# Kernel tuning notes

Measured on AMD Instinct MI355X. Metric: run time of the kernel, lower is better.

Reference implementation:

```python
import jax, jax.numpy as jnp
import numpy as np

N_HEADS = 16
N_KV = 8
HEAD_DIM = 128
HID = 2048
GROUPS = N_HEADS // N_KV
THETA = 10000.0


def _rope_cos_sin(position_ids, dtype):
    # position_ids: [1, S] int
    inv_freq = 1.0 / (THETA ** (jnp.arange(0, HEAD_DIM, 2, dtype=jnp.float32) / HEAD_DIM))
    freqs = position_ids.astype(jnp.float32)[:, :, None] * inv_freq[None, None, :]  # [1,S,hd/2]
    emb = jnp.concatenate([freqs, freqs], axis=-1)  # [1,S,hd]
    return jnp.cos(emb).astype(dtype)[:, None, :, :], jnp.sin(emb).astype(dtype)[:, None, :, :]


def _rotate_half(x):
    x1, x2 = x[..., : HEAD_DIM // 2], x[..., HEAD_DIM // 2 :]
    return jnp.concatenate([-x2, x1], axis=-1)


def setup_inputs() -> dict:
    key = jax.random.key(0)
    ks = jax.random.split(key, 8)
    B, S = 2, 2048
    hidden_states = jax.random.normal(ks[0], (B, S, HID), jnp.float32)
    Wq = jax.random.normal(ks[1], (HID, N_HEADS * HEAD_DIM), jnp.float32) * 0.02
    Wk = jax.random.normal(ks[2], (HID, N_KV * HEAD_DIM), jnp.float32) * 0.02
    Wv = jax.random.normal(ks[3], (HID, N_KV * HEAD_DIM), jnp.float32) * 0.02
    Wo = jax.random.normal(ks[4], (HID, HID), jnp.float32) * 0.02
    gate = jnp.zeros((1, N_HEADS, 1, 1), jnp.float32)
    memory_in = jax.random.normal(ks[5], (B, N_KV, HEAD_DIM, HEAD_DIM), jnp.float32)
    norm_in = jax.random.uniform(ks[6], (B, N_KV, 1, HEAD_DIM), jnp.float32)
    position_ids = jnp.arange(S, dtype=jnp.int32)[None, :]
    return {"hidden_states": hidden_states, "Wq": Wq, "Wk": Wk, "Wv": Wv, "Wo": Wo,
            "gate": gate, "memory_in": memory_in, "norm_in": norm_in,
            "position_ids": position_ids}


def reference(hidden_states, Wq, Wk, Wv, Wo, gate, memory_in, norm_in, position_ids):
    B, S, _ = hidden_states.shape
    # projections -> [B, H, S, hd]
    q = jnp.einsum('bsh,ho->bso', hidden_states, Wq).reshape(B, S, N_HEADS, HEAD_DIM).transpose(0, 2, 1, 3)
    k = jnp.einsum('bsh,ho->bso', hidden_states, Wk).reshape(B, S, N_KV, HEAD_DIM).transpose(0, 2, 1, 3)
    v = jnp.einsum('bsh,ho->bso', hidden_states, Wv).reshape(B, S, N_KV, HEAD_DIM).transpose(0, 2, 1, 3)

    # ---- compressive memory retrieval (pre-RoPE q, as in original) ----
    sigma_q = jax.nn.elu(q) + 1.0  # [B, nH, S, hd]
    mem_tiled = jnp.tile(memory_in, (1, GROUPS, 1, 1))          # torch .repeat tiles
    norm_tiled = jnp.tile(norm_in, (1, GROUPS, 1, 1))            # [B, nH, 1, hd]
    memory_output = jnp.einsum('bhsd,bhde->bhse', sigma_q, mem_tiled)
    norm_bcast = jnp.einsum('bhsd,bhd->bhs', sigma_q, norm_tiled[:, :, 0, :])[..., None]
    memory_output = memory_output / norm_bcast

    # ---- memory update (pre-RoPE k, v) ----
    sigma_k = jax.nn.elu(k) + 1.0  # [B, nKV, S, hd]
    updated_memory = memory_in + jnp.einsum('bhsd,bhse->bhde', sigma_k, v)
    updated_norm = norm_in + jnp.sum(sigma_k, axis=2, keepdims=True)

    # ---- RoPE ----
    cos, sin = _rope_cos_sin(position_ids, q.dtype)
    q = q * cos + _rotate_half(q) * sin
    k = k * cos + _rotate_half(k) * sin

    # ---- repeat_kv (interleave, groups) ----
    k = jnp.repeat(k, GROUPS, axis=1)
    v = jnp.repeat(v, GROUPS, axis=1)

    # ---- causal SDPA ----
    scale = 1.0 / np.sqrt(HEAD_DIM)
    scores = jnp.einsum('bhqd,bhkd->bhqk', q, k) * scale
    causal = jnp.tril(jnp.ones((S, S), dtype=bool))
    scores = jnp.where(causal[None, None], scores, jnp.finfo(scores.dtype).min)
    probs = jax.nn.softmax(scores, axis=-1)
    attn = jnp.einsum('bhqk,bhkd->bhqd', probs, v)

    # ---- gated combination + output projection ----
    g = jax.nn.sigmoid(gate)
    combined = g * memory_output + (1.0 - g) * attn  # [B, nH, S, hd]
    combined = combined.transpose(0, 2, 1, 3).reshape(B, S, HID)
    final_output = jnp.einsum('bsh,ho->bso', combined, Wo)
    return final_output, updated_memory, updated_norm
```

## Files before the change

kernel.cpp:

```cpp
#include <hip/hip_runtime.h>

#define BATCH 2
#define SEQ   2048
#define HID   2048
#define NH    16
#define NKV   8
#define HD    128
#define M_ROWS (BATCH * SEQ)
#define QKV_N  4096

typedef __attribute__((ext_vector_type(8))) __bf16 bf16x8;
typedef __attribute__((ext_vector_type(4))) float  f32x4;

static __device__ __forceinline__ f32x4 mfma16(bf16x8 a, bf16x8 b, f32x4 c) {
    return __builtin_amdgcn_mfma_f32_16x16x32_bf16(a, b, c, 0, 0, 0);
}
static __device__ __forceinline__ float sigma_f(float x) {
    return x > 0.f ? x + 1.f : __expf(x);
}
static __device__ __forceinline__ void gload16(const __bf16* g, __bf16* l) {
    __builtin_amdgcn_global_load_lds(
        (const __attribute__((address_space(1))) void*)g,
        (__attribute__((address_space(3))) void*)l, 16, 0, 0);
}

#define OFF_QKV  0ull
#define OFF_SQ   67108864ull
#define OFF_QR   83886080ull
#define OFF_KR   100663296ull
#define OFF_VT   109051904ull
#define OFF_ND   117440512ull
#define OFF_CB   117702656ull
#define OFF_PART 134479872ull
#define OFF_BND  142868480ull
#define OFF_MAXP 143130624ull
#define OFF_NPART 143134720ull
#define NSPLIT 8

__global__ void f2b_k(const float* __restrict__ src, __bf16* __restrict__ dst)
{
    const size_t i = ((size_t)blockIdx.x * 256 + threadIdx.x) * 8;
    const float4 v0 = *reinterpret_cast<const float4*>(src + i);
    const float4 v1 = *reinterpret_cast<const float4*>(src + i + 4);
    bf16x8 t;
    t[0]=(__bf16)v0.x; t[1]=(__bf16)v0.y; t[2]=(__bf16)v0.z; t[3]=(__bf16)v0.w;
    t[4]=(__bf16)v1.x; t[5]=(__bf16)v1.y; t[6]=(__bf16)v1.z; t[7]=(__bf16)v1.w;
    *reinterpret_cast<bf16x8*>(dst + i) = t;
}

__global__ __launch_bounds__(256) void tr_k(const float* __restrict__ W,
                                            __bf16* __restrict__ Bt, int K, int N)
{
    __shared__ __bf16 T[64][72];
    const int k0 = blockIdx.x * 64, n0 = blockIdx.y * 64;
    const int t = threadIdx.x;
    #pragma unroll
    for (int i = 0; i < 4; ++i) {
        const int idx = t + i * 256;
        const int r = idx >> 4, c4 = (idx & 15) * 4;
        const float4 v = *reinterpret_cast<const float4*>(&W[(size_t)(k0 + r) * N + n0 + c4]);
        T[c4 + 0][r] = (__bf16)v.x; T[c4 + 1][r] = (__bf16)v.y;
        T[c4 + 2][r] = (__bf16)v.z; T[c4 + 3][r] = (__bf16)v.w;
    }
    __syncthreads();
    #pragma unroll
    for (int i = 0; i < 2; ++i) {
        const int idx = t + i * 256;
        const int rr = idx >> 3, cc = (idx & 7) * 8;
        *reinterpret_cast<bf16x8*>(&Bt[(size_t)(n0 + rr) * K + k0 + cc]) =
            *reinterpret_cast<bf16x8*>(&T[rr][cc]);
    }
}

__global__ __launch_bounds__(512, 2) void gemm8_k(const __bf16* __restrict__ A,
                                                  const __bf16* __restrict__ Bt,
                                                  float* __restrict__ C,
                                                  int N, int K)
{
    __shared__ __align__(16) __bf16 smem[65536];
    const int tid = threadIdx.x, wave = tid >> 6, lane = tid & 63;
    const int l15 = lane & 15, l4 = lane >> 4;
    const int wr = wave >> 2, wc = wave & 3;

    const int nwg = gridDim.x;
    const int swz = (blockIdx.x & 7) * (nwg >> 3) + (blockIdx.x >> 3);
    const int NBN = N >> 8;
    const int bm = swz / NBN, bn = swz - bm * NBN;
    const int m0 = bm << 8, n0 = bn << 8;

    const int NKT = K >> 6;

    const int srow   = tid >> 2;
    const int schunk = (tid & 3) ^ ((tid >> 3) & 3);
    const int sdst   = wave * 512;

    const int achunk = l4 ^ ((l15 >> 1) & 3);
    const int aoff = (wr * 128 + l15) * 32 + achunk * 8;
    const int boff = (wc * 64  + l15) * 32 + achunk * 8;

    f32x4 acc[2][4][4] = {};
    bf16x8 af[4], bfr[4];

#define STAGE_SLAB(gb, r0, koff, slabptr) do {                                   \
        const __bf16* _g = (gb) + (size_t)((r0) + srow) * K + (koff) + schunk * 8; \
        gload16(_g,                    (slabptr) + sdst);                        \
        gload16(_g + (size_t)128 * K,  (slabptr) + sdst + 4096);                 \
    } while (0)

    STAGE_SLAB(A,  m0, 0,  smem);
    STAGE_SLAB(Bt, n0, 0,  smem + 16384);
    STAGE_SLAB(A,  m0, 32, smem + 8192);
    STAGE_SLAB(Bt, n0, 32, smem + 24576);
    STAGE_SLAB(A,  m0, 64, smem + 32768);
    STAGE_SLAB(Bt, n0, 64, smem + 32768 + 16384);
    asm volatile("s_waitcnt vmcnt(4)" ::: "memory");
    __builtin_amdgcn_s_barrier();

    #pragma unroll 1
    for (int T = 0; T < NKT; ++T) {
        __bf16* bufc = smem + (T & 1) * 32768;
        __bf16* bufn = smem + ((T & 1) ^ 1) * 32768;
        const int kt1 = (T + 1) * 64, kt2 = (T + 2) * 64;

        {
            const __bf16* As = bufc;
            const __bf16* Bs = bufc + 16384;
            #pragma unroll
            for (int f = 0; f < 4; ++f)  af[f]  = *reinterpret_cast<const bf16x8*>(As + aoff + f * 512);
            #pragma unroll
            for (int nf = 0; nf < 4; ++nf) bfr[nf] = *reinterpret_cast<const bf16x8*>(Bs + boff + nf * 512);
            if (T + 1 < NKT) STAGE_SLAB(A, m0, kt1 + 32, bufn + 8192);
            __builtin_amdgcn_s_barrier();
            __builtin_amdgcn_s_setprio(1);
            #pragma unroll
            for (int f = 0; f < 4; ++f)
                #pragma unroll
                for (int nf = 0; nf < 4; ++nf)
                    acc[0][f][nf] = mfma16(af[f], bfr[nf], acc[0][f][nf]);
            __builtin_amdgcn_s_setprio(0);
            __builtin_amdgcn_s_barrier();
        }
        {
            const __bf16* As = bufc;
            #pragma unroll
            for (int f = 0; f < 4; ++f)  af[f] = *reinterpret_cast<const bf16x8*>(As + aoff + 2048 + f * 512);
            if (T + 1 < NKT) STAGE_SLAB(Bt, n0, kt1 + 32, bufn + 24576);
            __builtin_amdgcn_s_barrier();
            __builtin_amdgcn_s_setprio(1);
            #pragma unroll
            for (int f = 0; f < 4; ++f)
                #pragma unroll
                for (int nf = 0; nf < 4; ++nf)
                    acc[1][f][nf] = mfma16(af[f], bfr[nf], acc[1][f][nf]);
            __builtin_amdgcn_s_setprio(0);
            __builtin_amdgcn_s_barrier();
        }
        {
            const __bf16* As = bufc + 8192;
            const __bf16* Bs = bufc + 24576;
            #pragma unroll
            for (int f = 0; f < 4; ++f)  af[f]  = *reinterpret_cast<const bf16x8*>(As + aoff + f * 512);
            #pragma unroll
            for (int nf = 0; nf < 4; ++nf) bfr[nf] = *reinterpret_cast<const bf16x8*>(Bs + boff + nf * 512);
            if (T + 2 < NKT) STAGE_SLAB(A, m0, kt2, bufc);
            __builtin_amdgcn_s_barrier();
            __builtin_amdgcn_s_setprio(1);
            #pragma unroll
            for (int f = 0; f < 4; ++f)
                #pragma unroll
                for (int nf = 0; nf < 4; ++nf)
                    acc[0][f][nf] = mfma16(af[f], bfr[nf], acc[0][f][nf]);
            __builtin_amdgcn_s_setprio(0);
            __builtin_amdgcn_s_barrier();
        }
        {
            const __bf16* As = bufc + 8192;
            #pragma unroll
            for (int f = 0; f < 4; ++f)  af[f] = *reinterpret_cast<const bf16x8*>(As + aoff + 2048 + f * 512);
            if (T + 2 < NKT) STAGE_SLAB(Bt, n0, kt2, bufc + 16384);
            __builtin_amdgcn_s_barrier();
            __builtin_amdgcn_s_setprio(1);
            #pragma unroll
            for (int f = 0; f < 4; ++f)
                #pragma unroll
                for (int nf = 0; nf < 4; ++nf)
                    acc[1][f][nf] = mfma16(af[f], bfr[nf], acc[1][f][nf]);
            __builtin_amdgcn_s_setprio(0);
            if (T < NKT - 2) asm volatile("s_waitcnt vmcnt(4)" ::: "memory");
            else             asm volatile("s_waitcnt vmcnt(0)" ::: "memory");
            __builtin_amdgcn_s_barrier();
        }
    }
#undef STAGE_SLAB

    #pragma unroll
    for (int mh = 0; mh < 2; ++mh)
        #pragma unroll
        for (int f = 0; f < 4; ++f)
            #pragma unroll
            for (int nf = 0; nf < 4; ++nf)
                #pragma unroll
                for (int r = 0; r < 4; ++r) {
                    const int row = m0 + wr * 128 + mh * 64 + f * 16 + l4 * 4 + r;
                    const int col = n0 + wc * 64 + nf * 16 + l15;
                    C[(size_t)row * N + col] = acc[mh][f][nf][r];
                }
}

__global__ __launch_bounds__(256) void prep_k(const float* __restrict__ qkv,
                                              const float* __restrict__ norm_in,
                                              const int* __restrict__ pos_ids,
                                              __bf16* __restrict__ sq, __bf16* __restrict__ qr,
                                              __bf16* __restrict__ kr, __bf16* __restrict__ vt,
                                              float* __restrict__ nd, float* __restrict__ bnd,
                                              float* __restrict__ maxp)
{
    const int sc = blockIdx.x, kvh = blockIdx.y, b = blockIdx.z;
    const int s0 = sc * 32, t = threadIdx.x;
    const float scale = 0.08838834764831845f;
    const float s2 = scale * scale;
    const float NEG_LN_TH = -0.14391156831212787f;
    __shared__ float krn[32];

    {
        const int row = t >> 2;
        const int head = row >> 5, sl = row & 31;
        const int hq = kvh * 2 + head, nh = hq & 7;
        const int dq = (t & 3) * 16;
        const int pos = pos_ids[s0 + sl];
        const float* qp = qkv + (size_t)(b * SEQ + s0 + sl) * QKV_N + hq * 128;
        const float* np = norm_in + (b * NKV + nh) * 128;

        float x0[16], x1[16];
        #pragma unroll
        for (int i = 0; i < 16; i += 4) {
            *reinterpret_cast<float4*>(&x0[i]) = *reinterpret_cast<const float4*>(qp + dq + i);
            *reinterpret_cast<float4*>(&x1[i]) = *reinterpret_cast<const float4*>(qp + dq + 64 + i);
        }
        float nds = 0.f, qns = 0.f;
        bf16x8 sqv0[2], sqv1[2], qrv0[2], qrv1[2];
        #pragma unroll
        for (int i = 0; i < 16; ++i) {
            const int j = dq + i;
            float c, sn;
            __sincosf((float)pos * __expf((float)j * NEG_LN_TH), &sn, &c);
            qrv0[i >> 3][i & 7] = (__bf16)((x0[i] * c - x1[i] * sn) * scale);
            qrv1[i >> 3][i & 7] = (__bf16)((x1[i] * c + x0[i] * sn) * scale);
            const float sg0 = sigma_f(x0[i]), sg1 = sigma_f(x1[i]);
            sqv0[i >> 3][i & 7] = (__bf16)sg0;
            sqv1[i >> 3][i & 7] = (__bf16)sg1;
            nds += sg0 * np[j] + sg1 * np[j + 64];
            qns += (x0[i] * x0[i] + x1[i] * x1[i]) * s2;
        }
        __bf16* sqp = sq + ((size_t)(b * NH + hq) * SEQ + s0 + sl) * 128;
        __bf16* qrp = qr + ((size_t)(b * NH + hq) * SEQ + s0 + sl) * 128;
        *reinterpret_cast<bf16x8*>(sqp + dq)      = sqv0[0];
        *reinterpret_cast<bf16x8*>(sqp + dq + 8)  = sqv0[1];
        *reinterpret_cast<bf16x8*>(sqp + dq + 64) = sqv1[0];
        *reinterpret_cast<bf16x8*>(sqp + dq + 72) = sqv1[1];
        *reinterpret_cast<bf16x8*>(qrp + dq)      = qrv0[0];
        *reinterpret_cast<bf16x8*>(qrp + dq + 8)  = qrv0[1];
        *reinterpret_cast<bf16x8*>(qrp + dq + 64) = qrv1[0];
        *reinterpret_cast<bf16x8*>(qrp + dq + 72) = qrv1[1];

        nds += __shfl_xor(nds, 1); nds += __shfl_xor(nds, 2);
        qns += __shfl_xor(qns, 1); qns += __shfl_xor(qns, 2);
        if ((t & 3) == 0) {
            nd [(size_t)(b * NH + hq) * SEQ + s0 + sl] = nds;
            bnd[(size_t)(b * NH + hq) * SEQ + s0 + sl] = qns;
        }
    }

    if (t < 128) {
        const int sl = t >> 2;
        const int dq = (t & 3) * 16;
        const int pos = pos_ids[s0 + sl];
        const float* kp = qkv + (size_t)(b * SEQ + s0 + sl) * QKV_N + 2048 + kvh * 128;
        float x0[16], x1[16];
        #pragma unroll
        for (int i = 0; i < 16; i += 4) {
            *reinterpret_cast<float4*>(&x0[i]) = *reinterpret_cast<const float4*>(kp + dq + i);
            *reinterpret_cast<float4*>(&x1[i]) = *reinterpret_cast<const float4*>(kp + dq + 64 + i);
        }
        bf16x8 kv0[2], kv1[2];
        float kns = 0.f;
        #pragma unroll
        for (int i = 0; i < 16; ++i) {
            const int j = dq + i;
            float c, sn;
            __sincosf((float)pos * __expf((float)j * NEG_LN_TH), &sn, &c);
            kv0[i >> 3][i & 7] = (__bf16)(x0[i] * c - x1[i] * sn);
            kv1[i >> 3][i & 7] = (__bf16)(x1[i] * c + x0[i] * sn);
            kns += x0[i] * x0[i] + x1[i] * x1[i];
        }
        __bf16* krp = kr + ((size_t)(b * NKV + kvh) * SEQ + s0 + sl) * 128;
        *reinterpret_cast<bf16x8*>(krp + dq)      = kv0[0];
        *reinterpret_cast<bf16x8*>(krp + dq + 8)  = kv0[1];
        *reinterpret_cast<bf16x8*>(krp + dq + 64) = kv1[0];
        *reinterpret_cast<bf16x8*>(krp + dq + 72) = kv1[1];
        kns += __shfl_xor(kns, 1); kns += __shfl_xor(kns, 2);
        if ((t & 3) == 0) krn[sl] = kns;
    }

    __shared__ float vl[128][33];
    {
        const int sl = t >> 3, dch = (t & 7) * 16;
        const float* vp = qkv + (size_t)(b * SEQ + s0 + sl) * QKV_N + 3072 + kvh * 128 + dch;
        float xv[16];
        #pragma unroll
        for (int i = 0; i < 16; i += 4)
            *reinterpret_cast<float4*>(&xv[i]) = *reinterpret_cast<const float4*>(vp + i);
        #pragma unroll
        for (int i = 0; i < 16; ++i) vl[dch + i][sl] = xv[i];
    }
    __syncthreads();
    if (t == 0) {
        float mx = 0.f;
        #pragma unroll
        for (int i = 0; i < 32; ++i) mx = fmaxf(mx, krn[i]);
        maxp[((b * NKV + kvh) << 6) + sc] = mx;
    }
    {
        const int d = t >> 1, sh = (t & 1) * 16;
        bf16x8 o0, o1;
        #pragma unroll
        for (int j = 0; j < 8; ++j) o0[j] = (__bf16)vl[d][sh + j];
        #pragma unroll
        for (int j = 0; j < 8; ++j) o1[j] = (__bf16)vl[d][sh + 8 + j];
        __bf16* vp = vt + ((size_t)((b * NKV + kvh) * 128 + d)) * SEQ + s0 + sh;
        *reinterpret_cast<bf16x8*>(vp)     = o0;
        *reinterpret_cast<bf16x8*>(vp + 8) = o1;
    }
}

__global__ __launch_bounds__(256) void memout_k(const __bf16* __restrict__ sq,
                                                const float* __restrict__ mem_in,
                                                const float* __restrict__ nd,
                                                const float* __restrict__ gate,
                                                __bf16* __restrict__ cb)
{
    __shared__ __align__(16) __bf16 mt[128][136];
    const int tid = threadIdx.x;
    const int h = blockIdx.y, b = blockIdx.z;
    const int s0 = blockIdx.x * 64;

    const float* mem = mem_in + (size_t)(b * NKV + (h & 7)) * 16384;
    for (int i = tid; i < 16384; i += 256) {
        int dd = i >> 7, e = i & 127;
        mt[e][dd] = (__bf16)mem[i];
    }
    __syncthreads();

    const int wave = tid >> 6, lane = tid & 63, l15 = lane & 15, l4 = lane >> 4;
    f32x4 acc[8] = {};
    const __bf16* sqb = sq + ((size_t)(b * NH + h) * SEQ + s0 + wave * 16 + l15) * 128;
    #pragma unroll
    for (int kb = 0; kb < 4; ++kb) {
        bf16x8 a = *reinterpret_cast<const bf16x8*>(sqb + kb * 32 + l4 * 8);
        #pragma unroll
        for (int nc = 0; nc < 8; ++nc) {
            bf16x8 bb = *reinterpret_cast<bf16x8*>(&mt[nc * 16 + l15][kb * 32 + l4 * 8]);
            acc[nc] = mfma16(a, bb, acc[nc]);
        }
    }
    float g = 1.f / (1.f + __expf(-gate[h]));
    #pragma unroll
    for (int r = 0; r < 4; ++r) {
        int srow = s0 + wave * 16 + l4 * 4 + r;
        float scl = g / nd[(size_t)(b * NH + h) * SEQ + srow];
        __bf16* cbp = cb + (size_t)(b * SEQ + srow) * HID + h * 128;
        #pragma unroll
        for (int nc = 0; nc < 8; ++nc)
            cbp[nc * 16 + l15] = (__bf16)(acc[nc][r] * scl);
    }
}

__global__ __launch_bounds__(256) void memupd_k(const float* __restrict__ qkv,
                                                float* __restrict__ part,
                                                float* __restrict__ npart)
{
    const int sp = blockIdx.x, h = blockIdx.y, b = blockIdx.z;
    const int tid = threadIdx.x;
    const int tx = tid & 15, ty = tid >> 4;
    __shared__ __align__(16) float sk[8][128];
    __shared__ __align__(16) float sv[8][128];
    float acc[8][8] = {};
    float nacc = 0.f;

    const int s0 = sp * (SEQ / NSPLIT);
    for (int so = 0; so < SEQ / NSPLIT; so += 8) {
        for (int i = tid; i < 8 * 128; i += 256) {
            int rr = i >> 7, dd = i & 127;
            const float* rowp = qkv + (size_t)(b * SEQ + s0 + so + rr) * QKV_N;
            sk[rr][dd] = sigma_f(rowp[2048 + h * 128 + dd]);
            sv[rr][dd] = rowp[3072 + h * 128 + dd];
        }
        __syncthreads();
        if (tid < 128) {
            #pragma unroll
            for (int rr = 0; rr < 8; ++rr) nacc += sk[rr][tid];
        }
        #pragma unroll
        for (int rr = 0; rr < 8; ++rr) {
            float4 k0 = *reinterpret_cast<float4*>(&sk[rr][tx * 8]);
            float4 k1 = *reinterpret_cast<float4*>(&sk[rr][tx * 8 + 4]);
            float4 v0 = *reinterpret_cast<float4*>(&sv[rr][ty * 8]);
            float4 v1 = *reinterpret_cast<float4*>(&sv[rr][ty * 8 + 4]);
            float kreg[8] = {k0.x,k0.y,k0.z,k0.w,k1.x,k1.y,k1.z,k1.w};
            float vreg[8] = {v0.x,v0.y,v0.z,v0.w,v1.x,v1.y,v1.z,v1.w};
            #pragma unroll
            for (int i = 0; i < 8; ++i)
                #pragma unroll
                for (int j2 = 0; j2 < 8; ++j2)
                    acc[i][j2] += kreg[i] * vreg[j2];
        }
        __syncthreads();
    }
    float* pb = part + ((size_t)sp * (BATCH * NKV) + b * NKV + h) * 16384;
    #pragma unroll
    for (int i = 0; i < 8; ++i)
        #pragma unroll
        for (int j2 = 0; j2 < 8; ++j2)
            pb[(tx * 8 + i) * 128 + ty * 8 + j2] = acc[i][j2];
    if (tid < 128)
        npart[((size_t)sp * (BATCH * NKV) + b * NKV + h) * 128 + tid] = nacc;
}

__global__ void memred_k(const float* __restrict__ part, const float* __restrict__ mem_in,
                         float* __restrict__ out_mem)
{
    const size_t i = (size_t)blockIdx.x * 256 + threadIdx.x;
    float a = mem_in[i];
    #pragma unroll
    for (int sp = 0; sp < NSPLIT; ++sp) a += part[(size_t)sp * 262144 + i];
    out_mem[i] = a;
}

__global__ void normred_k(const float* __restrict__ npart, const float* __restrict__ norm_in,
                          float* __restrict__ out_norm)
{
    const int bh = blockIdx.x, d = threadIdx.x;
    float a = norm_in[bh * 128 + d];
    #pragma unroll
    for (int sp = 0; sp < NSPLIT; ++sp)
        a += npart[((size_t)sp * (BATCH * NKV) + bh) * 128 + d];
    out_norm[bh * 128 + d] = a;
}

__global__ __launch_bounds__(256, 2) void attn_k(const __bf16* __restrict__ qr,
                                                 const __bf16* __restrict__ kr,
                                                 const __bf16* __restrict__ vt,
                                                 const float* __restrict__ gate,
                                                 const float* __restrict__ bnd,
                                                 const float* __restrict__ maxp,
                                                 __bf16* __restrict__ cb)
{
    __shared__ __align__(16) char smem[81920];
    char* ksB = smem;
    char* vsB = smem + 32768;
    char* pB  = smem + 65536;
    float*  red  = (float*)smem;
    float*  lred = (float*)(smem + 65536);

    const int tid = threadIdx.x, wave = tid >> 6, lane = tid & 63;
    const int l15 = lane & 15, l4 = lane >> 4;
    const int e3 = l15 & 7, e2 = e3 >> 2;
    const int ksub = wave >> 1;
    const int wq   = wave & 1;

    const int n   = blockIdx.x + 16 * (blockIdx.y + 16 * blockIdx.z);
    const int xcd = n & 7, i64 = n >> 3;
    const int grp = xcd * 2 + (i64 >> 5);
    const int within = i64 & 31;
    const int b   = grp >> 3;
    const int kvh = grp & 7;
    const int h   = kvh * 2 + (within >> 4);
    const int x   = within & 15;

    const __bf16* kbase = kr + (size_t)(b * NKV + kvh) * SEQ * 128;
    const __bf16* vbase = vt + (size_t)(b * NKV + kvh) * 128 * SEQ;
    const float* bbase  = bnd + (size_t)(b * NH + h) * SEQ;

    const float g  = 1.f / (1.f + __expf(-gate[h]));
    const float gi = 1.f - g;
    float kn2 = 0.f;
    const float* mp = maxp + (b * NKV + kvh) * 64;
    #pragma unroll
    for (int i = 0; i < 64; i += 4) {
        const float4 v = *reinterpret_cast<const float4*>(mp + i);
        kn2 = fmaxf(kn2, fmaxf(fmaxf(v.x, v.y), fmaxf(v.z, v.w)));
    }
    const float knmax = sqrtf(kn2);

    bf16x8 ones;
    #pragma unroll
    for (int j = 0; j < 8; ++j) ones[j] = (__bf16)1.0f;

    const int srow = wave * 32 + l4;
    const int chA  = (lane & 15) ^ l4;
    const char* KG0 = (const char*)kbase + srow * 256 + chA * 16;
    const char* KG1 = (const char*)kbase + srow * 256 + ((chA ^ 4) * 16);
    const char* VG0 = (const char*)vbase + srow * 4096 + chA * 16;
    const char* VG1 = (const char*)vbase + srow * 4096 + ((chA ^ 4) * 16);
    __bf16* kdst = (__bf16*)(ksB + wave * 8192);
    __bf16* vdst = (__bf16*)(vsB + wave * 8192);

    const int t16 = (l4 ^ (e3 & 3)) * 16;
    const int KBe = l15 * 256 + ksub * 16384 + t16 + e2 * 64;
    const int KBo = l15 * 256 + ksub * 16384 + t16 + (1 ^ e2) * 64;
    const int VB0 = l15 * 256 + t16 + e2 * 64 + ksub * 128;
    const int VB1 = l15 * 256 + t16 + (1 ^ e2) * 64 + ksub * 128;
    const int PWw = wave * 4096 + l4 * 512 + l15 * 2;
    const int PWr = wave * 4096 + l15 * 128 + l4 * 16;

#define ISSUE_K(ktrow) do {                                                      \
        const int _ko = (ktrow) * 256;                                           \
        _Pragma("unroll")                                                        \
        for (int _j = 0; _j < 8; ++_j)                                           \
            gload16((const __bf16*)(((_j & 1) ? KG1 : KG0) + _ko + _j * 1024),   \
                    kdst + _j * 512);                                            \
    } while (0)
#define ISSUE_V(ktrow) do {                                                      \
        const int _vo = (ktrow) * 2;                                             \
        _Pragma("unroll")                                                        \
        for (int _j = 0; _j < 8; ++_j)                                           \
            gload16((const __bf16*)(((_j & 1) ? VG1 : VG0) + _vo + _j * 16384),  \
                    vdst + _j * 512);                                            \
    } while (0)

    #pragma unroll 1
    for (int tile = 0; tile < 2; ++tile) {
        const int q0 = (tile == 0 ? x : 31 - x) * 64;
        const int qw = q0 + wq * 32;
        const int NT = (q0 >> 6) + 1;
        const int NI = (NT + 1) >> 1;

        bf16x8 af[2][4];
        float m_r[2][4];
        #pragma unroll
        for (int m = 0; m < 2; ++m) {
            const __bf16* qb = qr + ((size_t)(b * NH + h) * SEQ + qw + m * 16 + l15) * 128;
            #pragma unroll
            for (int kb = 0; kb < 4; ++kb)
                af[m][kb] = *reinterpret_cast<const bf16x8*>(qb + kb * 32 + l4 * 8);
            #pragma unroll
            for (int r = 0; r < 4; ++r)
                m_r[m][r] = sqrtf(bbase[qw + m * 16 + l4 * 4 + r]) * knmax + 1.0f;
        }

        f32x4 o0[8] = {}, o1[8] = {};
        f32x4 lc0 = {}, lc1 = {};

        ISSUE_K(0);
        ISSUE_V(0);
        asm volatile("s_waitcnt vmcnt(8)" ::: "memory");
        __builtin_amdgcn_sched_barrier(0);
        __builtin_amdgcn_s_barrier();

        #pragma unroll 1
        for (int it = 0; it < NI; ++it) {
            const int s = 2 * it + ksub;
            const bool act  = (s < NT);
            const bool more = (it + 1 < NI);

            f32x4 s0[4] = {}, s1[4] = {};
            if (act) {
                __builtin_amdgcn_s_setprio(1);
                #pragma unroll
                for (int kb = 0; kb < 4; ++kb) {
                    const int kbb = ((kb & 1) ? KBo : KBe) + (kb >> 1) * 128;
                    #pragma unroll
                    for (int sub = 0; sub < 4; ++sub) {
                        bf16x8 bb = *reinterpret_cast<const bf16x8*>(ksB + kbb + sub * 4096);
                        s0[sub] = mfma16(af[0][kb], bb, s0[sub]);
                        s1[sub] = mfma16(af[1][kb], bb, s1[sub]);
                    }
                }
                __builtin_amdgcn_s_setprio(0);
            }
            __builtin_amdgcn_sched_barrier(0);
            __builtin_amdgcn_s_barrier();

            if (more) ISSUE_K((it + 1) * 128);

            if (act) {
                #pragma unroll
                for (int r = 0; r < 4; ++r) {
                    const int q0r = qw + l4 * 4 + r;
                    const int q1r = q0r + 16;
                    #pragma unroll
                    for (int sub = 0; sub < 4; ++sub) {
                        const int key = s * 64 + sub * 16 + l15;
                        float p0 = __expf(s0[sub][r] - m_r[0][r]);
                        float p1 = __expf(s1[sub][r] - m_r[1][r]);
                        p0 = (key <= q0r) ? p0 : 0.f;
                        p1 = (key <= q1r) ? p1 : 0.f;
                        *(__bf16*)(pB + PWw + r * 128 + sub * 32)        = (__bf16)p0;
                        *(__bf16*)(pB + PWw + 2048 + r * 128 + sub * 32) = (__bf16)p1;
                    }
                }
            }
            if (more) asm volatile("s_waitcnt vmcnt(8)" ::: "memory");
            else      asm volatile("s_waitcnt vmcnt(0)" ::: "memory");
            __builtin_amdgcn_sched_barrier(0);
            __builtin_amdgcn_s_barrier();

            if (act) {
                bf16x8 a00 = *reinterpret_cast<const bf16x8*>(pB + PWr);
                bf16x8 a01 = *reinterpret_cast<const bf16x8*>(pB + PWr + 64);
                bf16x8 a10 = *reinterpret_cast<const bf16x8*>(pB + PWr + 2048);
                bf16x8 a11 = *reinterpret_cast<const bf16x8*>(pB + PWr + 2048 + 64);
                __builtin_amdgcn_s_setprio(1);
                lc0 = mfma16(a00, ones, lc0); lc0 = mfma16(a01, ones, lc0);
                lc1 = mfma16(a10, ones, lc1); lc1 = mfma16(a11, ones, lc1);
                #pragma unroll
                for (int nc = 0; nc < 8; ++nc) {
                    bf16x8 b0 = *reinterpret_cast<const bf16x8*>(vsB + VB0 + nc * 4096);
                    bf16x8 b1 = *reinterpret_cast<const bf16x8*>(vsB + VB1 + nc * 4096);
                    o0[nc] = mfma16(a00, b0, o0[nc]); o0[nc] = mfma16(a01, b1, o0[nc]);
                    o1[nc] = mfma16(a10, b0, o1[nc]); o1[nc] = mfma16(a11, b1, o1[nc]);
                }
                __builtin_amdgcn_s_setprio(0);
            }
            __builtin_amdgcn_sched_barrier(0);
            __builtin_amdgcn_s_barrier();

            if (more) {
                ISSUE_V((it + 1) * 128);
                asm volatile("s_waitcnt vmcnt(8)" ::: "memory");
            } else {
                asm volatile("s_waitcnt vmcnt(0)" ::: "memory");
            }
            __builtin_amdgcn_sched_barrier(0);
            __builtin_amdgcn_s_barrier();
        }

        if (wave >= 2) {
            float* rb = red + (wave - 2) * 4224;
            #pragma unroll
            for (int nc = 0; nc < 8; ++nc)
                #pragma unroll
                for (int r = 0; r < 4; ++r) {
                    rb[(l4 * 4 + r) * 132 + nc * 16 + l15]        = o0[nc][r];
                    rb[(16 + l4 * 4 + r) * 132 + nc * 16 + l15]   = o1[nc][r];
                }
            if (l15 == 0) {
                float* lb = lred + (wave - 2) * 32;
                #pragma unroll
                for (int r = 0; r < 4; ++r) {
                    lb[l4 * 4 + r]      = lc0[r];
                    lb[16 + l4 * 4 + r] = lc1[r];
                }
            }
        }
        __syncthreads();
        if (wave < 2) {
            float* rb = red + wave * 4224;
            const float* lb = lred + wave * 32;
            #pragma unroll
            for (int r = 0; r < 4; ++r) {
                const int qrow = qw + l4 * 4 + r;
                const float i0 = gi / (lc0[r] + lb[l4 * 4 + r]);
                const float i1 = gi / (lc1[r] + lb[16 + l4 * 4 + r]);
                __bf16* c0 = cb + (size_t)(b * SEQ + qrow) * HID + h * 128;
                __bf16* c1 = cb + (size_t)(b * SEQ + qrow + 16) * HID + h * 128;
                #pragma unroll
                for (int nc = 0; nc < 8; ++nc) {
                    const int dd = nc * 16 + l15;
                    const float v0 = o0[nc][r] + rb[(l4 * 4 + r) * 132 + dd];
                    const float v1 = o1[nc][r] + rb[(16 + l4 * 4 + r) * 132 + dd];
                    c0[dd] = (__bf16)((float)c0[dd] + v0 * i0);
                    c1[dd] = (__bf16)((float)c1[dd] + v1 * i1);
                }
            }
        }
        __syncthreads();
    }
#undef ISSUE_K
#undef ISSUE_V
}

extern "C" void kernel_launch(void* const* d_in, const int* in_sizes, int n_in,
                              void* d_out, int out_size, void* d_ws, size_t ws_size,
                              hipStream_t stream)
{
    const float* hidden  = (const float*)d_in[0];
    const float* Wq      = (const float*)d_in[1];
    const float* Wk      = (const float*)d_in[2];
    const float* Wv      = (const float*)d_in[3];
    const float* Wo      = (const float*)d_in[4];
    const float* gate    = (const float*)d_in[5];
    const float* mem_in  = (const float*)d_in[6];
    const float* norm_in = (const float*)d_in[7];
    const int*   pos     = (const int*)d_in[8];

    float* out_final = (float*)d_out;
    float* out_mem   = out_final + (size_t)BATCH * SEQ * HID;
    float* out_norm  = out_mem + (size_t)BATCH * NKV * 128 * 128;

    char* ws = (char*)d_ws;
    float*  qkv  = (float*)(ws + OFF_QKV);
    __bf16* sq   = (__bf16*)(ws + OFF_SQ);
    __bf16* qrb  = (__bf16*)(ws + OFF_QR);
    __bf16* krb  = (__bf16*)(ws + OFF_KR);
    __bf16* vtb  = (__bf16*)(ws + OFF_VT);
    float*  nd   = (float*)(ws + OFF_ND);
    __bf16* cb   = (__bf16*)(ws + OFF_CB);
    float*  part = (float*)(ws + OFF_PART);
    float*  bnd  = (float*)(ws + OFF_BND);
    float*  maxp = (float*)(ws + OFF_MAXP);
    float*  npart = (float*)(ws + OFF_NPART);
    __bf16* hb   = (__bf16*)(ws + OFF_SQ);
    __bf16* qkvT = (__bf16*)(ws + OFF_QR);
    __bf16* woT  = (__bf16*)(ws + OFF_PART);

    f2b_k<<<(M_ROWS * HID) / (256 * 8), 256, 0, stream>>>(hidden, hb);
    tr_k<<<dim3(HID / 64, 2048 / 64), 256, 0, stream>>>(Wq, qkvT, HID, 2048);
    tr_k<<<dim3(HID / 64, 1024 / 64), 256, 0, stream>>>(Wk, qkvT + (size_t)2048 * HID, HID, 1024);
    tr_k<<<dim3(HID / 64, 1024 / 64), 256, 0, stream>>>(Wv, qkvT + (size_t)3072 * HID, HID, 1024);

    gemm8_k<<<(M_ROWS / 256) * (QKV_N / 256), 512, 0, stream>>>(hb, qkvT, qkv, QKV_N, HID);

    prep_k<<<dim3(SEQ / 32, NKV, BATCH), 256, 0, stream>>>(qkv, norm_in, pos, sq, qrb, krb, vtb,
                                                           nd, bnd, maxp);

    memout_k<<<dim3(SEQ / 64, NH, BATCH), 256, 0, stream>>>(sq, mem_in, nd, gate, cb);

    memupd_k<<<dim3(NSPLIT, NKV, BATCH), 256, 0, stream>>>(qkv, part, npart);
    memred_k<<<(BATCH * NKV * 128 * 128) / 256, 256, 0, stream>>>(part, mem_in, out_mem);
    normred_k<<<BATCH * NKV, 128, 0, stream>>>(npart, norm_in, out_norm);

    tr_k<<<dim3(HID / 64, HID / 64), 256, 0, stream>>>(Wo, woT, HID, HID);

    attn_k<<<dim3(16, NH, BATCH), 256, 0, stream>>>(qrb, krb, vtb, gate, bnd, maxp, cb);

    gemm8_k<<<(M_ROWS / 256) * (HID / 256), 512, 0, stream>>>(cb, woT, out_final, HID, HID);
}
```

Before: 470.3 us.

## Merge prep kernels, swizzle P tile in LDS, add smaller-tile output GEMM

Folds the hidden-state bf16 conversion and the three weight transposes into one launch, and merges the memory and norm reductions into another, cutting kernel launches. Applies an XOR swizzle to the attention probability tile in LDS to reduce bank conflicts on writes and reads. Replaces the output projection GEMM with a 128x256 tile variant with a blockIdx swizzle, double-buffered LDS and 2 blocks per CU, so the grid has more workgroups for better CU occupancy. The new GEMM adds another hand-written pipeline with waitcnt-based synchronisation that has to be correct.

```diff
diff --git a/kernel.cpp b/kernel.cpp
--- a/kernel.cpp
+++ b/kernel.cpp
@@ -37,15 +37,48 @@
 #define OFF_NPART 143134720ull
 #define NSPLIT 8
 
-__global__ void f2b_k(const float* __restrict__ src, __bf16* __restrict__ dst)
-{
-    const size_t i = ((size_t)blockIdx.x * 256 + threadIdx.x) * 8;
-    const float4 v0 = *reinterpret_cast<const float4*>(src + i);
-    const float4 v1 = *reinterpret_cast<const float4*>(src + i + 4);
-    bf16x8 t;
-    t[0]=(__bf16)v0.x; t[1]=(__bf16)v0.y; t[2]=(__bf16)v0.z; t[3]=(__bf16)v0.w;
-    t[4]=(__bf16)v1.x; t[5]=(__bf16)v1.y; t[6]=(__bf16)v1.z; t[7]=(__bf16)v1.w;
-    *reinterpret_cast<bf16x8*>(dst + i) = t;
+__global__ __launch_bounds__(256) void pre_k(const float* __restrict__ hidden,
+                                             const float* __restrict__ Wq,
+                                             const float* __restrict__ Wk,
+                                             const float* __restrict__ Wv,
+                                             __bf16* __restrict__ hb,
+                                             __bf16* __restrict__ qkvT)
+{
+    __shared__ __bf16 T[64][72];
+    const int bid = blockIdx.x;
+    const int t = threadIdx.x;
+    if (bid < 4096) {
+        const size_t i = ((size_t)bid * 256 + t) * 8;
+        const float4 v0 = *reinterpret_cast<const float4*>(hidden + i);
+        const float4 v1 = *reinterpret_cast<const float4*>(hidden + i + 4);
+        bf16x8 o;
+        o[0]=(__bf16)v0.x; o[1]=(__bf16)v0.y; o[2]=(__bf16)v0.z; o[3]=(__bf16)v0.w;
+        o[4]=(__bf16)v1.x; o[5]=(__bf16)v1.y; o[6]=(__bf16)v1.z; o[7]=(__bf16)v1.w;
+        *reinterpret_cast<bf16x8*>(hb + i) = o;
+        return;
+    }
+    int tb = bid - 4096;
+    const float* W; __bf16* Bt; int N;
+    if (tb < 1024)      { W = Wq; Bt = qkvT;                         N = 2048; }
+    else if (tb < 1536) { W = Wk; Bt = qkvT + (size_t)2048 * HID;    N = 1024; tb -= 1024; }
+    else                { W = Wv; Bt = qkvT + (size_t)3072 * HID;    N = 1024; tb -= 1536; }
+    const int k0 = (tb & 31) * 64, n0 = (tb >> 5) * 64;
+    #pragma unroll
+    for (int i = 0; i < 4; ++i) {
+        const int idx = t + i * 256;
+        const int r = idx >> 4, c4 = (idx & 15) * 4;
+        const float4 v = *reinterpret_cast<const float4*>(&W[(size_t)(k0 + r) * N + n0 + c4]);
+        T[c4 + 0][r] = (__bf16)v.x; T[c4 + 1][r] = (__bf16)v.y;
+        T[c4 + 2][r] = (__bf16)v.z; T[c4 + 3][r] = (__bf16)v.w;
+    }
+    __syncthreads();
+    #pragma unroll
+    for (int i = 0; i < 2; ++i) {
+        const int idx = t + i * 256;
+        const int rr = idx >> 3, cc = (idx & 7) * 8;
+        *reinterpret_cast<bf16x8*>(&Bt[(size_t)(n0 + rr) * HID + k0 + cc]) =
+            *reinterpret_cast<bf16x8*>(&T[rr][cc]);
+    }
 }
 
 __global__ __launch_bounds__(256) void tr_k(const float* __restrict__ W,
@@ -205,6 +238,109 @@
                     const int col = n0 + wc * 64 + nf * 16 + l15;
                     C[(size_t)row * N + col] = acc[mh][f][nf][r];
                 }
+}
+
+__global__ __launch_bounds__(512, 2) void gemm8n_k(const __bf16* __restrict__ A,
+                                                   const __bf16* __restrict__ Bt,
+                                                   float* __restrict__ C,
+                                                   int N, int K)
+{
+    __shared__ __align__(16) __bf16 smem[49152];
+    const int tid = threadIdx.x, wave = tid >> 6, lane = tid & 63;
+    const int l15 = lane & 15, l4 = lane >> 4;
+    const int wr = wave >> 2, wc = wave & 3;
+
+    const int nwg = gridDim.x;
+    const int swz = (blockIdx.x & 7) * (nwg >> 3) + (blockIdx.x >> 3);
+    const int NBN = N >> 8;
+    const int bm = swz / NBN, bn = swz - bm * NBN;
+    const int m0 = bm << 7, n0 = bn << 8;
+
+    const int NKT = K >> 6;
+
+    const int srow   = tid >> 2;
+    const int schunk = (tid & 3) ^ ((tid >> 3) & 3);
+    const int sdst   = wave * 512;
+
+    const int achunk = l4 ^ ((l15 >> 1) & 3);
+    const int aoff = (wr * 64 + l15) * 32 + achunk * 8;
+    const int boff = (wc * 64 + l15) * 32 + achunk * 8;
+
+    f32x4 acc[4][4] = {};
+    bf16x8 af[4], bfr[4];
+
+#define STAGE_A(koff, dstp) do {                                                  \
+        gload16(A + (size_t)(m0 + srow) * K + (koff) + schunk * 8, (dstp) + sdst); \
+    } while (0)
+#define STAGE_B(koff, dstp) do {                                                  \
+        const __bf16* _g = Bt + (size_t)(n0 + srow) * K + (koff) + schunk * 8;    \
+        gload16(_g,                   (dstp) + sdst);                             \
+        gload16(_g + (size_t)128 * K, (dstp) + sdst + 4096);                      \
+    } while (0)
+
+    STAGE_A(0,  smem);
+    STAGE_B(0,  smem + 8192);
+    STAGE_A(32, smem + 4096);
+    STAGE_B(32, smem + 16384);
+    STAGE_A(64, smem + 24576);
+    STAGE_B(64, smem + 24576 + 8192);
+    asm volatile("s_waitcnt vmcnt(3)" ::: "memory");
+    __builtin_amdgcn_s_barrier();
+
+    #pragma unroll 1
+    for (int T = 0; T < NKT; ++T) {
+        __bf16* bufc = smem + (T & 1) * 24576;
+        __bf16* bufn = smem + ((T & 1) ^ 1) * 24576;
+        const int kt1 = (T + 1) * 64, kt2 = (T + 2) * 64;
+
+        {
+            #pragma unroll
+            for (int f = 0; f < 4; ++f)  af[f]  = *reinterpret_cast<const bf16x8*>(bufc + aoff + f * 512);
+            #pragma unroll
+            for (int nf = 0; nf < 4; ++nf) bfr[nf] = *reinterpret_cast<const bf16x8*>(bufc + 8192 + boff + nf * 512);
+            if (T + 1 < NKT) { STAGE_A(kt1 + 32, bufn + 4096); STAGE_B(kt1 + 32, bufn + 16384); }
+            __builtin_amdgcn_s_barrier();
+            __builtin_amdgcn_s_setprio(1);
+            #pragma unroll
+            for (int f = 0; f < 4; ++f)
+                #pragma unroll
+                for (int nf = 0; nf < 4; ++nf)
+                    acc[f][nf] = mfma16(af[f], bfr[nf], acc[f][nf]);
+            __builtin_amdgcn_s_setprio(0);
+            __builtin_amdgcn_s_barrier();
+        }
+        {
+            #pragma unroll
+            for (int f = 0; f < 4; ++f)  af[f]  = *reinterpret_cast<const bf16x8*>(bufc + 4096 + aoff + f * 512);
+            #pragma unroll
+            for (int nf = 0; nf < 4; ++nf) bfr[nf] = *reinterpret_cast<const bf16x8*>(bufc + 16384 + boff + nf * 512);
+            if (T + 2 < NKT) { STAGE_A(kt2, bufc); STAGE_B(kt2, bufc + 8192); }
+            __builtin_amdgcn_s_barrier();
+            __builtin_amdgcn_s_setprio(1);
+            #pragma unroll
+            for (int f = 0; f < 4; ++f)
+                #pragma unroll
+                for (int nf = 0; nf < 4; ++nf)
+                    acc[f][nf] = mfma16(af[f], bfr[nf], acc[f][nf]);
+            __builtin_amdgcn_s_setprio(0);
+            if (T < NKT - 2) asm volatile("s_waitcnt vmcnt(3)" ::: "memory");
+            else             asm volatile("s_waitcnt vmcnt(0)" ::: "memory");
+            __builtin_amdgcn_s_barrier();
+        }
+    }
+#undef STAGE_A
+#undef STAGE_B
+
+    #pragma unroll
+    for (int f = 0; f < 4; ++f)
+        #pragma unroll
+        for (int nf = 0; nf < 4; ++nf)
+            #pragma unroll
+            for (int r = 0; r < 4; ++r) {
+                const int row = m0 + wr * 64 + f * 16 + l4 * 4 + r;
+                const int col = n0 + wc * 64 + nf * 16 + l15;
+                C[(size_t)row * N + col] = acc[f][nf][r];
+            }
 }
 
 __global__ __launch_bounds__(256) void prep_k(const float* __restrict__ qkv,
@@ -426,25 +562,28 @@
         npart[((size_t)sp * (BATCH * NKV) + b * NKV + h) * 128 + tid] = nacc;
 }
 
-__global__ void memred_k(const float* __restrict__ part, const float* __restrict__ mem_in,
-                         float* __restrict__ out_mem)
-{
-    const size_t i = (size_t)blockIdx.x * 256 + threadIdx.x;
-    float a = mem_in[i];
-    #pragma unroll
-    for (int sp = 0; sp < NSPLIT; ++sp) a += part[(size_t)sp * 262144 + i];
-    out_mem[i] = a;
-}
-
-__global__ void normred_k(const float* __restrict__ npart, const float* __restrict__ norm_in,
-                          float* __restrict__ out_norm)
-{
-    const int bh = blockIdx.x, d = threadIdx.x;
-    float a = norm_in[bh * 128 + d];
-    #pragma unroll
-    for (int sp = 0; sp < NSPLIT; ++sp)
-        a += npart[((size_t)sp * (BATCH * NKV) + bh) * 128 + d];
-    out_norm[bh * 128 + d] = a;
+__global__ __launch_bounds__(256) void memrednorm_k(const float* __restrict__ part,
+                                                    const float* __restrict__ mem_in,
+                                                    float* __restrict__ out_mem,
+                                                    const float* __restrict__ npart,
+                                                    const float* __restrict__ norm_in,
+                                                    float* __restrict__ out_norm)
+{
+    const int bid = blockIdx.x;
+    if (bid < 1024) {
+        const size_t i = (size_t)bid * 256 + threadIdx.x;
+        float a = mem_in[i];
+        #pragma unroll
+        for (int sp = 0; sp < NSPLIT; ++sp) a += part[(size_t)sp * 262144 + i];
+        out_mem[i] = a;
+    } else if (threadIdx.x < 128) {
+        const int bh = bid - 1024, d = threadIdx.x;
+        float a = norm_in[bh * 128 + d];
+        #pragma unroll
+        for (int sp = 0; sp < NSPLIT; ++sp)
+            a += npart[((size_t)sp * (BATCH * NKV) + bh) * 128 + d];
+        out_norm[bh * 128 + d] = a;
+    }
 }
 
 __global__ __launch_bounds__(256, 2) void attn_k(const __bf16* __restrict__ qr,
@@ -510,8 +649,8 @@
     const int KBo = l15 * 256 + ksub * 16384 + t16 + (1 ^ e2) * 64;
     const int VB0 = l15 * 256 + t16 + e2 * 64 + ksub * 128;
     const int VB1 = l15 * 256 + t16 + (1 ^ e2) * 64 + ksub * 128;
-    const int PWw = wave * 4096 + l4 * 512 + l15 * 2;
-    const int PWr = wave * 4096 + l15 * 128 + l4 * 16;
+    const int PWb = wave * 4096 + (l15 & 7) * 2;
+    const int PR  = wave * 4096 + l15 * 128 + ((l4 ^ e3) * 16);
 
 #define ISSUE_K(ktrow) do {                                                      \
         const int _ko = (ktrow) * 256;                                           \
@@ -588,6 +727,8 @@
                 for (int r = 0; r < 4; ++r) {
                     const int q0r = qw + l4 * 4 + r;
                     const int q1r = q0r + 16;
+                    const int p0r = l4 * 4 + r;
+                    const int rw0 = PWb + p0r * 128;
                     #pragma unroll
                     for (int sub = 0; sub < 4; ++sub) {
                         const int key = s * 64 + sub * 16 + l15;
@@ -595,8 +736,9 @@
                         float p1 = __expf(s1[sub][r] - m_r[1][r]);
                         p0 = (key <= q0r) ? p0 : 0.f;
                         p1 = (key <= q1r) ? p1 : 0.f;
-                        *(__bf16*)(pB + PWw + r * 128 + sub * 32)        = (__bf16)p0;
-                        *(__bf16*)(pB + PWw + 2048 + r * 128 + sub * 32) = (__bf16)p1;
+                        const int cc = (sub * 2 + (l15 >> 3)) ^ (p0r & 7);
+                        *(__bf16*)(pB + rw0 + cc * 16)        = (__bf16)p0;
+                        *(__bf16*)(pB + rw0 + cc * 16 + 2048) = (__bf16)p1;
                     }
                 }
             }
@@ -606,10 +748,10 @@
             __builtin_amdgcn_s_barrier();
 
             if (act) {
-                bf16x8 a00 = *reinterpret_cast<const bf16x8*>(pB + PWr);
-                bf16x8 a01 = *reinterpret_cast<const bf16x8*>(pB + PWr + 64);
-                bf16x8 a10 = *reinterpret_cast<const bf16x8*>(pB + PWr + 2048);
-                bf16x8 a11 = *reinterpret_cast<const bf16x8*>(pB + PWr + 2048 + 64);
+                bf16x8 a00 = *reinterpret_cast<const bf16x8*>(pB + PR);
+                bf16x8 a01 = *reinterpret_cast<const bf16x8*>(pB + (PR ^ 64));
+                bf16x8 a10 = *reinterpret_cast<const bf16x8*>(pB + PR + 2048);
+                bf16x8 a11 = *reinterpret_cast<const bf16x8*>(pB + (PR ^ 64) + 2048);
                 __builtin_amdgcn_s_setprio(1);
                 lc0 = mfma16(a00, ones, lc0); lc0 = mfma16(a01, ones, lc0);
                 lc1 = mfma16(a10, ones, lc1); lc1 = mfma16(a11, ones, lc1);
@@ -714,10 +856,7 @@
     __bf16* qkvT = (__bf16*)(ws + OFF_QR);
     __bf16* woT  = (__bf16*)(ws + OFF_PART);
 
-    f2b_k<<<(M_ROWS * HID) / (256 * 8), 256, 0, stream>>>(hidden, hb);
-    tr_k<<<dim3(HID / 64, 2048 / 64), 256, 0, stream>>>(Wq, qkvT, HID, 2048);
-    tr_k<<<dim3(HID / 64, 1024 / 64), 256, 0, stream>>>(Wk, qkvT + (size_t)2048 * HID, HID, 1024);
-    tr_k<<<dim3(HID / 64, 1024 / 64), 256, 0, stream>>>(Wv, qkvT + (size_t)3072 * HID, HID, 1024);
+    pre_k<<<6144, 256, 0, stream>>>(hidden, Wq, Wk, Wv, hb, qkvT);
 
     gemm8_k<<<(M_ROWS / 256) * (QKV_N / 256), 512, 0, stream>>>(hb, qkvT, qkv, QKV_N, HID);
 
@@ -727,12 +866,11 @@
     memout_k<<<dim3(SEQ / 64, NH, BATCH), 256, 0, stream>>>(sq, mem_in, nd, gate, cb);
 
     memupd_k<<<dim3(NSPLIT, NKV, BATCH), 256, 0, stream>>>(qkv, part, npart);
-    memred_k<<<(BATCH * NKV * 128 * 128) / 256, 256, 0, stream>>>(part, mem_in, out_mem);
-    normred_k<<<BATCH * NKV, 128, 0, stream>>>(npart, norm_in, out_norm);
+    memrednorm_k<<<1040, 256, 0, stream>>>(part, mem_in, out_mem, npart, norm_in, out_norm);
 
     tr_k<<<dim3(HID / 64, HID / 64), 256, 0, stream>>>(Wo, woT, HID, HID);
 
     attn_k<<<dim3(16, NH, BATCH), 256, 0, stream>>>(qrb, krb, vtb, gate, bnd, maxp, cb);
 
-    gemm8_k<<<(M_ROWS / 256) * (HID / 256), 512, 0, stream>>>(cb, woT, out_final, HID, HID);
-}
+    gemm8n_k<<<(M_ROWS / 128) * (HID / 256), 512, 0, stream>>>(cb, woT, out_final, HID, HID);
+}
```

After: 440.1 us. -6.4%, faster.
